# Performance work log

Measured on AMD Instinct MI355X. Metric: run time of the kernel, lower is better.

The kernel has to match this reference:

```python
import jax, jax.numpy as jnp
import numpy as np

DECAY = 0.99
EPS = 1e-05


def setup_inputs() -> dict:
    key = jax.random.key(0)
    k1, k2, k3, k4 = jax.random.split(key, 4)
    B, D, T, E = 16, 64, 4096, 1024
    x = jax.random.normal(k1, (B, D, T), dtype=jnp.float32)
    embedding = jax.random.uniform(k2, (E, D), dtype=jnp.float32,
                                   minval=-1.0 / E, maxval=1.0 / E)
    ema_size = jax.random.uniform(k3, (E,), dtype=jnp.float32)
    ema_w = jax.random.normal(k4, (D, E), dtype=jnp.float32)
    return {"x": x, "embedding": embedding, "ema_size": ema_size, "ema_w": ema_w}


def reference(x, embedding, ema_size, ema_w):
    # x: [B, D, T] (bdt_flag=True -> transpose to [B, T, D])
    B, D, T = x.shape
    E = embedding.shape[0]
    xt = jnp.swapaxes(x, 1, 2)                      # [B, T, D]
    flat = xt.reshape(-1, D)                        # [B*T, D]
    dist = (jnp.sum(embedding * embedding, axis=1)[None, :]
            - 2.0 * flat @ embedding.T
            + jnp.sum(flat * flat, axis=1, keepdims=True))  # [B*T, E]
    quantized_idx = jnp.argmin(dist, axis=1).reshape(B, T)   # [B, T] int
    onehot = jax.nn.one_hot(quantized_idx, E, dtype=x.dtype)  # [B, T, E]
    embed_idx = onehot @ embedding                  # [B, T, D]  (old codebook)
    # --- EMA codebook update (training branch) ---
    new_ema_size = DECAY * ema_size + (1.0 - DECAY) * jnp.sum(
        onehot.reshape(-1, E), axis=0)
    embed_sum = jnp.einsum('btd,bte->de', xt, onehot)        # [D, E]
    new_ema_w = DECAY * ema_w + (1.0 - DECAY) * embed_sum
    n = jnp.sum(new_ema_size)
    new_ema_size = (new_ema_size + EPS) / (n + E * EPS) * n
    new_embedding = (new_ema_w / new_ema_size[None, :]).T    # [E, D]
    # straight-through estimator
    embed_idx_qx = xt + jax.lax.stop_gradient(embed_idx - xt)
    embed_idx_qx = jnp.swapaxes(embed_idx_qx, 1, 2)          # back to [B, D, T]
    return embed_idx, embed_idx_qx, quantized_idx, new_embedding, new_ema_size, new_ema_w
```

## Files before the change

kernel.cpp:

```cpp
#include <hip/hip_runtime.h>
#include <hip/hip_bf16.h>

constexpr int Bc = 16, Dc = 64, Tc = 4096, Ec = 1024;
constexpr int NROW = Bc * Tc;
constexpr float DECAYF = 0.99f;
constexpr float OMDF   = 0.01f;
constexpr float EPSF   = 1e-5f;

typedef short bf16x8 __attribute__((ext_vector_type(8)));
typedef float f32x4  __attribute__((ext_vector_type(4)));

constexpr size_t O_EI  = 0;
constexpr size_t O_QX  = 4194304;
constexpr size_t O_IDX = 8388608;
constexpr size_t O_EMB = 8454144;
constexpr size_t O_ESZ = 8519680;
constexpr size_t O_EMW = 8520704;

constexpr size_t S_XH = 0;
constexpr size_t S_XM = 2097152;
constexpr size_t S_XL = 4194304;
constexpr size_t S_EH = 6291456;
constexpr size_t S_EM = 6324224;
constexpr size_t S_EL = 6356992;
constexpr size_t S_E2 = 6389760;
constexpr size_t S_X2 = 6424576;
constexpr size_t S_P  = 6557696;


__device__ inline unsigned short bf16bits(float v) {
  union { __hip_bfloat16 b; unsigned short u; } c;
  c.b = __float2bfloat16(v);
  return c.u;
}
__device__ inline float bf16val(unsigned short u) {
  union { unsigned u32; float f; } c;
  c.u32 = ((unsigned)u) << 16;
  return c.f;
}
__device__ inline void split3(float x, unsigned short& h, unsigned short& m,
                              unsigned short& l) {
  h = bf16bits(x);
  float r1 = x - bf16val(h);
  m = bf16bits(r1);
  float r2 = r1 - bf16val(m);
  l = bf16bits(r2);
}

__device__ inline void pack8(unsigned short* s, uint4* dst) {
  uint4 v;
  v.x = (unsigned)s[0] | ((unsigned)s[1] << 16);
  v.y = (unsigned)s[2] | ((unsigned)s[3] << 16);
  v.z = (unsigned)s[4] | ((unsigned)s[5] << 16);
  v.w = (unsigned)s[6] | ((unsigned)s[7] << 16);
  *dst = v;
}

__device__ inline void gl_lds16(const unsigned short* g, unsigned short* l) {
  __builtin_amdgcn_global_load_lds(
      (const __attribute__((address_space(1))) void*)g,
      (__attribute__((address_space(3))) void*)l, 16, 0, 0);
}

__global__ __launch_bounds__(256) void decomp_x(const float* __restrict__ x,
                                                float* __restrict__ out) {
  const int row = blockIdx.x * 256 + threadIdx.x;
  const int b = row >> 12, t = row & (Tc - 1);
  const float* xrow = x + (size_t)b * Dc * Tc + t;
  float xv[64];
  #pragma unroll
  for (int d = 0; d < Dc; ++d) xv[d] = xrow[(size_t)d * Tc];

  float x2;
  {
    #pragma clang fp contract(off)
    float r[8];
    #pragma unroll
    for (int j = 0; j < 8; ++j) r[j] = xv[j] * xv[j];
    #pragma unroll
    for (int k = 1; k < 8; ++k) {
      #pragma unroll
      for (int j = 0; j < 8; ++j) r[j] += xv[8 * k + j] * xv[8 * k + j];
    }
    x2 = ((r[0] + r[1]) + (r[2] + r[3])) + ((r[4] + r[5]) + (r[6] + r[7]));
  }
  out[S_X2 + row] = x2;

  uint4* ph = (uint4*)((unsigned short*)(out + S_XH) + (size_t)row * 64);
  uint4* pm = (uint4*)((unsigned short*)(out + S_XM) + (size_t)row * 64);
  uint4* pl = (uint4*)((unsigned short*)(out + S_XL) + (size_t)row * 64);
  #pragma unroll
  for (int k = 0; k < 8; ++k) {
    unsigned short hs[8], ms[8], ls[8];
    #pragma unroll
    for (int j = 0; j < 8; ++j) split3(xv[8 * k + j], hs[j], ms[j], ls[j]);
    pack8(hs, ph + k); pack8(ms, pm + k); pack8(ls, pl + k);
  }
}

__global__ __launch_bounds__(256) void decomp_e(const float* __restrict__ emb,
                                                float* __restrict__ out,
                                                float* __restrict__ ws) {
  const int c = blockIdx.x * 256 + threadIdx.x;
  if (c < 1024) ws[c] = 0.0f;
  if (c >= Ec) return;
  const float* ep = emb + (size_t)c * Dc;
  float ev[64];
  #pragma unroll
  for (int d = 0; d < Dc; ++d) ev[d] = ep[d];

  float e2;
  {
    #pragma clang fp contract(off)
    float r[8];
    #pragma unroll
    for (int j = 0; j < 8; ++j) r[j] = ev[j] * ev[j];
    #pragma unroll
    for (int k = 1; k < 8; ++k) {
      #pragma unroll
      for (int j = 0; j < 8; ++j) r[j] += ev[8 * k + j] * ev[8 * k + j];
    }
    e2 = ((r[0] + r[1]) + (r[2] + r[3])) + ((r[4] + r[5]) + (r[6] + r[7]));
  }
  out[S_E2 + c] = e2;

  uint4* ph = (uint4*)((unsigned short*)(out + S_EH) + (size_t)c * 64);
  uint4* pm = (uint4*)((unsigned short*)(out + S_EM) + (size_t)c * 64);
  uint4* pl = (uint4*)((unsigned short*)(out + S_EL) + (size_t)c * 64);
  #pragma unroll
  for (int k = 0; k < 8; ++k) {
    unsigned short hs[8], ms[8], ls[8];
    #pragma unroll
    for (int j = 0; j < 8; ++j) split3(ev[8 * k + j], hs[j], ms[j], ls[j]);
    pack8(hs, ph + k); pack8(ms, pm + k); pack8(ls, pl + k);
  }
}

constexpr int TW = 64;
constexpr int SLOTS = (TW / 16) * 3 * 2 * 64;

__global__ __launch_bounds__(512)
__attribute__((amdgpu_waves_per_eu(2, 2)))
void gemm_argmin(float* __restrict__ out) {
  __shared__ alignas(16) unsigned short lbuf[2][SLOTS * 8];

  const int tid  = threadIdx.x;
  const int lane = tid & 63;
  const int wave = tid >> 6;
  const int col  = lane & 15;
  const int quad = lane >> 4;
  const int rowbase = blockIdx.x * 256 + wave * 32;

  const unsigned short* XH = (const unsigned short*)(out + S_XH);
  const unsigned short* XM = (const unsigned short*)(out + S_XM);
  const unsigned short* XL = (const unsigned short*)(out + S_XL);
  const unsigned short* EHu = (const unsigned short*)(out + S_EH);
  const float* E2 = out + S_E2;
  const float* X2 = out + S_X2;

  auto stage = [&](int tl, int s) {
    #pragma unroll
    for (int i = 0; i < 3; ++i) {
      int slot = tid + i * 512;
      int sl   = slot & 63;
      int sub  = slot >> 6;
      int half = sub & 1;
      int pl   = (sub >> 1) % 3;
      int nt   = sub / 6;
      int cw   = tl * TW + nt * 16 + (sl & 15);
      int q    = sl >> 4;
      const unsigned short* src =
          EHu + (size_t)pl * 65536 + (size_t)cw * 64 + half * 32 + q * 8;
      gl_lds16(src, &lbuf[s][(size_t)slot * 8]);
    }
  };

  bf16x8 a[12];
  #pragma unroll
  for (int mt = 0; mt < 2; ++mt) {
    size_t ao = (size_t)(rowbase + mt * 16 + col) * 64 + quad * 8;
    a[mt * 6 + 0] = *(const bf16x8*)(XH + ao);
    a[mt * 6 + 1] = *(const bf16x8*)(XH + ao + 32);
    a[mt * 6 + 2] = *(const bf16x8*)(XM + ao);
    a[mt * 6 + 3] = *(const bf16x8*)(XM + ao + 32);
    a[mt * 6 + 4] = *(const bf16x8*)(XL + ao);
    a[mt * 6 + 5] = *(const bf16x8*)(XL + ao + 32);
  }
  float x2v[8];
  #pragma unroll
  for (int mt = 0; mt < 2; ++mt)
    #pragma unroll
    for (int r = 0; r < 4; ++r)
      x2v[mt * 4 + r] = X2[rowbase + mt * 16 + quad * 4 + r];

  #pragma unroll
  for (int i = 0; i < 12; ++i) asm volatile("" : "+v"(a[i]));
  #pragma unroll
  for (int i = 0; i < 8; ++i) asm volatile("" : "+v"(x2v[i]));

  float best[8];
  int bidx[8];
  #pragma unroll
  for (int i = 0; i < 8; ++i) { best[i] = 3.4e38f; bidx[i] = 0; }

  stage(0, 0);

  for (int tl = 0; tl < Ec / TW; ++tl) {
    __syncthreads();
    if (tl + 1 < Ec / TW) stage(tl + 1, (tl + 1) & 1);
    const unsigned short* lb = lbuf[tl & 1];

    #pragma unroll
    for (int np = 0; np < 2; ++np) {
      bf16x8 b0[6], b1[6];
      #pragma unroll
      for (int pl = 0; pl < 3; ++pl)
        #pragma unroll
        for (int h = 0; h < 2; ++h) {
          b0[pl * 2 + h] = *(const bf16x8*)(
              lb + ((size_t)(((((2 * np + 0) * 3 + pl) * 2 + h)) * 64 + lane)) * 8);
          b1[pl * 2 + h] = *(const bf16x8*)(
              lb + ((size_t)(((((2 * np + 1) * 3 + pl) * 2 + h)) * 64 + lane)) * 8);
        }
      const float e2v0 = E2[tl * TW + (2 * np + 0) * 16 + col];
      const float e2v1 = E2[tl * TW + (2 * np + 1) * 16 + col];

      f32x4 acc00 = {0.f, 0.f, 0.f, 0.f};
      f32x4 acc01 = {0.f, 0.f, 0.f, 0.f};
      f32x4 acc10 = {0.f, 0.f, 0.f, 0.f};
      f32x4 acc11 = {0.f, 0.f, 0.f, 0.f};
      const int PA[6] = {0, 0, 1, 1, 0, 2};
      const int PB[6] = {0, 1, 0, 1, 2, 0};
      #pragma unroll
      for (int p = 0; p < 6; ++p) {
        #pragma unroll
        for (int s = 0; s < 2; ++s) {
          bf16x8 a0 = a[PA[p] * 2 + s];
          bf16x8 a1 = a[6 + PA[p] * 2 + s];
          bf16x8 f0 = b0[PB[p] * 2 + s];
          bf16x8 f1 = b1[PB[p] * 2 + s];
          acc00 = __builtin_amdgcn_mfma_f32_16x16x32_bf16(a0, f0, acc00, 0, 0, 0);
          acc10 = __builtin_amdgcn_mfma_f32_16x16x32_bf16(a0, f1, acc10, 0, 0, 0);
          acc01 = __builtin_amdgcn_mfma_f32_16x16x32_bf16(a1, f0, acc01, 0, 0, 0);
          acc11 = __builtin_amdgcn_mfma_f32_16x16x32_bf16(a1, f1, acc11, 0, 0, 0);
        }
      }

      const int cw0 = tl * TW + (2 * np + 0) * 16 + col;
      const int cw1 = tl * TW + (2 * np + 1) * 16 + col;
      #pragma unroll
      for (int r = 0; r < 4; ++r) {
        {
          float q = __builtin_fmaf(-2.0f, acc00[r], e2v0);
          q = q + x2v[r];
          if (q < best[r]) { best[r] = q; bidx[r] = cw0; }
        }
        {
          float q = __builtin_fmaf(-2.0f, acc01[r], e2v0);
          q = q + x2v[4 + r];
          if (q < best[4 + r]) { best[4 + r] = q; bidx[4 + r] = cw0; }
        }
        {
          float q = __builtin_fmaf(-2.0f, acc10[r], e2v1);
          q = q + x2v[r];
          if (q < best[r]) { best[r] = q; bidx[r] = cw1; }
        }
        {
          float q = __builtin_fmaf(-2.0f, acc11[r], e2v1);
          q = q + x2v[4 + r];
          if (q < best[4 + r]) { best[4 + r] = q; bidx[4 + r] = cw1; }
        }
      }
    }
  }

  #pragma unroll
  for (int i = 0; i < 8; ++i) {
    float bq = best[i];
    int bi = bidx[i];
    #pragma unroll
    for (int m = 1; m <= 8; m <<= 1) {
      float qo = __shfl_xor(bq, m, 64);
      int io = __shfl_xor(bi, m, 64);
      bool take = (qo < bq) || (qo == bq && io < bi);
      bq = take ? qo : bq;
      bi = take ? io : bi;
    }
    if (col == 0) {
      int mt = i >> 2, r = i & 3;
      int row = rowbase + mt * 16 + quad * 4 + r;
      out[O_IDX + row] = (float)bi;
    }
  }
}

__global__ __launch_bounds__(512) void esum_partial(float* __restrict__ out,
                                                    float* __restrict__ ws) {
  const int c = blockIdx.x;
  const int s = blockIdx.y;
  __shared__ float acc[4 * 1025];
  __shared__ float cnt[1024];
  for (int i = threadIdx.x; i < 4 * 1025; i += 512) acc[i] = 0.f;
  if (s == 0)
    for (int i = threadIdx.x; i < 1024; i += 512) cnt[i] = 0.f;
  __syncthreads();

  const unsigned short* XH = (const unsigned short*)(out + S_XH);
  const unsigned short* XM = (const unsigned short*)(out + S_XM);
  const unsigned short* XL = (const unsigned short*)(out + S_XL);

  #pragma unroll 2
  for (int it = 0; it < 8; ++it) {
    const int r = c * 4096 + it * 512 + threadIdx.x;
    const int bi = (int)out[O_IDX + r];
    const size_t off = (size_t)r * 64 + s * 4;
    const uint2 h = *(const uint2*)(XH + off);
    const uint2 m = *(const uint2*)(XM + off);
    const uint2 l = *(const uint2*)(XL + off);

#define DOPAIR(k, HW, MW, LW)                                                  \
    {                                                                          \
      float v0 = (bf16val((unsigned short)(HW)) +                              \
                  bf16val((unsigned short)(MW))) +                             \
                 bf16val((unsigned short)(LW));                                \
      float v1 = (bf16val((unsigned short)((HW) >> 16)) +                      \
                  bf16val((unsigned short)((MW) >> 16))) +                     \
                 bf16val((unsigned short)((LW) >> 16));                        \
      atomicAdd(&acc[(2 * (k) + 0) * 1025 + bi], v0);                          \
      atomicAdd(&acc[(2 * (k) + 1) * 1025 + bi], v1);                          \
    }
    DOPAIR(0, h.x, m.x, l.x)
    DOPAIR(1, h.y, m.y, l.y)
#undef DOPAIR
    if (s == 0) atomicAdd(&cnt[bi], 1.0f);
  }
  __syncthreads();

  float* part = out + S_P + ((size_t)c * 64 + s * 4) * 1024;
  for (int i = threadIdx.x; i < 4096; i += 512)
    part[i] = acc[(i >> 10) * 1025 + (i & 1023)];
  if (s == 0)
    for (int i = threadIdx.x; i < 1024; i += 512)
      atomicAdd(&ws[i], cnt[i]);
}

__global__ __launch_bounds__(1024) void finalize_a(
    const float* __restrict__ ema_size, float* __restrict__ ws,
    float* __restrict__ out) {
  const int e = threadIdx.x;
  float ns = DECAYF * ema_size[e] + OMDF * ws[e];
  __shared__ float red[1024];
  red[e] = ns;
  __syncthreads();
  for (int s = 512; s > 0; s >>= 1) {
    if (e < s) red[e] += red[e + s];
    __syncthreads();
  }
  float n = red[0];
  float v = ((ns + EPSF) / (n + (float)Ec * EPSF)) * n;
  out[O_ESZ + e] = v;
  ws[66560 + e] = v;
}

__global__ __launch_bounds__(256) void esum_finalize_w(
    const float* __restrict__ ema_w, const float* __restrict__ ws,
    float* __restrict__ out) {
  const int i = blockIdx.x * 256 + threadIdx.x;
  float v = 0.f;
  #pragma unroll
  for (int c = 0; c < 16; ++c) v += out[S_P + (size_t)c * 65536 + i];
  int d = i >> 10;
  int e = i & (Ec - 1);
  float w = DECAYF * ema_w[i] + OMDF * v;
  out[O_EMW + i] = w;
  out[O_EMB + e * Dc + d] = w / ws[66560 + e];
}

__global__ __launch_bounds__(256) void epilogue_kernel(
    const float* __restrict__ x, const float* __restrict__ emb,
    float* __restrict__ out) {
  const int row = blockIdx.x * 256 + threadIdx.x;
  const int b = row >> 12, t = row & (Tc - 1);
  const float* xrow = x + (size_t)b * Dc * Tc + t;

  const int bi = (int)out[O_IDX + row];

  const float4* eb = (const float4*)(emb + (size_t)bi * Dc);
  float* qx_base = out + O_QX + (size_t)b * Dc * Tc + t;
  float4* ei_base = (float4*)(out + O_EI + (size_t)row * Dc);

  #pragma unroll
  for (int k = 0; k < 16; ++k) {
    float4 ev = eb[k];
    ei_base[k] = ev;
    {
      const int d = 4 * k + 0; float xd = xrow[(size_t)d * Tc];
      float diff = ev.x - xd;
      qx_base[(size_t)d * Tc] = xd + diff;
    }
    {
      const int d = 4 * k + 1; float xd = xrow[(size_t)d * Tc];
      float diff = ev.y - xd;
      qx_base[(size_t)d * Tc] = xd + diff;
    }
    {
      const int d = 4 * k + 2; float xd = xrow[(size_t)d * Tc];
      float diff = ev.z - xd;
      qx_base[(size_t)d * Tc] = xd + diff;
    }
    {
      const int d = 4 * k + 3; float xd = xrow[(size_t)d * Tc];
      float diff = ev.w - xd;
      qx_base[(size_t)d * Tc] = xd + diff;
    }
  }
}

extern "C" void kernel_launch(void* const* d_in, const int* in_sizes, int n_in,
                              void* d_out, int out_size, void* d_ws, size_t ws_size,
                              hipStream_t stream) {
  const float* x        = (const float*)d_in[0];
  const float* emb      = (const float*)d_in[1];
  const float* ema_size = (const float*)d_in[2];
  const float* ema_w    = (const float*)d_in[3];
  float* out = (float*)d_out;
  float* ws  = (float*)d_ws;

  decomp_x<<<NROW / 256, 256, 0, stream>>>(x, out);
  decomp_e<<<Ec / 256, 256, 0, stream>>>(emb, out, ws);
  gemm_argmin<<<NROW / 256, 512, 0, stream>>>(out);
  esum_partial<<<dim3(16, 16), 512, 0, stream>>>(out, ws);
  finalize_a<<<1, 1024, 0, stream>>>(ema_size, ws, out);
  esum_finalize_w<<<Ec * Dc / 256, 256, 0, stream>>>(ema_w, ws, out);
  epilogue_kernel<<<NROW / 256, 256, 0, stream>>>(x, emb, out);
}
```

Measured before the change: 187.8 us.

## Load codebook fragments directly from global into registers, dropping LDS staging

The argmin GEMM no longer stages codebook tiles into double-buffered shared memory through global_load_lds and block barriers. Each wave now loads its B fragments straight from global (L2-resident) memory into registers, with a one-step register prefetch. The block size is halved to 256 threads with 128 rows per block, so there are twice as many blocks. This removes the barriers and the LDS traffic, but every wave now reads the codebook itself, and register pressure rises from the prefetch buffers.

```diff
diff --git a/kernel.cpp b/kernel.cpp
--- a/kernel.cpp
+++ b/kernel.cpp
@@ -56,12 +56,6 @@
   *dst = v;
 }
 
-__device__ inline void gl_lds16(const unsigned short* g, unsigned short* l) {
-  __builtin_amdgcn_global_load_lds(
-      (const __attribute__((address_space(1))) void*)g,
-      (__attribute__((address_space(3))) void*)l, 16, 0, 0);
-}
-
 __global__ __launch_bounds__(256) void decomp_x(const float* __restrict__ x,
                                                 float* __restrict__ out) {
   const int row = blockIdx.x * 256 + threadIdx.x;
@@ -136,20 +130,15 @@
   }
 }
 
-constexpr int TW = 64;
-constexpr int SLOTS = (TW / 16) * 3 * 2 * 64;
-
-__global__ __launch_bounds__(512)
+__global__ __launch_bounds__(256)
 __attribute__((amdgpu_waves_per_eu(2, 2)))
 void gemm_argmin(float* __restrict__ out) {
-  __shared__ alignas(16) unsigned short lbuf[2][SLOTS * 8];
-
   const int tid  = threadIdx.x;
   const int lane = tid & 63;
   const int wave = tid >> 6;
   const int col  = lane & 15;
   const int quad = lane >> 4;
-  const int rowbase = blockIdx.x * 256 + wave * 32;
+  const int rowbase = blockIdx.x * 128 + wave * 32;
 
   const unsigned short* XH = (const unsigned short*)(out + S_XH);
   const unsigned short* XM = (const unsigned short*)(out + S_XM);
@@ -158,22 +147,7 @@
   const float* E2 = out + S_E2;
   const float* X2 = out + S_X2;
 
-  auto stage = [&](int tl, int s) {
-    #pragma unroll
-    for (int i = 0; i < 3; ++i) {
-      int slot = tid + i * 512;
-      int sl   = slot & 63;
-      int sub  = slot >> 6;
-      int half = sub & 1;
-      int pl   = (sub >> 1) % 3;
-      int nt   = sub / 6;
-      int cw   = tl * TW + nt * 16 + (sl & 15);
-      int q    = sl >> 4;
-      const unsigned short* src =
-          EHu + (size_t)pl * 65536 + (size_t)cw * 64 + half * 32 + q * 8;
-      gl_lds16(src, &lbuf[s][(size_t)slot * 8]);
-    }
-  };
+  const unsigned short* Bbase = EHu + (size_t)col * 64 + (size_t)quad * 8;
 
   bf16x8 a[12];
   #pragma unroll
@@ -203,74 +177,78 @@
   #pragma unroll
   for (int i = 0; i < 8; ++i) { best[i] = 3.4e38f; bidx[i] = 0; }
 
-  stage(0, 0);
-
-  for (int tl = 0; tl < Ec / TW; ++tl) {
-    __syncthreads();
-    if (tl + 1 < Ec / TW) stage(tl + 1, (tl + 1) & 1);
-    const unsigned short* lb = lbuf[tl & 1];
-
-    #pragma unroll
-    for (int np = 0; np < 2; ++np) {
-      bf16x8 b0[6], b1[6];
+  auto loadB = [&](int it, bf16x8* b0, bf16x8* b1) {
+    const unsigned short* p = Bbase + (size_t)it * 2048;
+    #pragma unroll
+    for (int pl = 0; pl < 3; ++pl)
       #pragma unroll
-      for (int pl = 0; pl < 3; ++pl)
-        #pragma unroll
-        for (int h = 0; h < 2; ++h) {
-          b0[pl * 2 + h] = *(const bf16x8*)(
-              lb + ((size_t)(((((2 * np + 0) * 3 + pl) * 2 + h)) * 64 + lane)) * 8);
-          b1[pl * 2 + h] = *(const bf16x8*)(
-              lb + ((size_t)(((((2 * np + 1) * 3 + pl) * 2 + h)) * 64 + lane)) * 8);
-        }
-      const float e2v0 = E2[tl * TW + (2 * np + 0) * 16 + col];
-      const float e2v1 = E2[tl * TW + (2 * np + 1) * 16 + col];
-
-      f32x4 acc00 = {0.f, 0.f, 0.f, 0.f};
-      f32x4 acc01 = {0.f, 0.f, 0.f, 0.f};
-      f32x4 acc10 = {0.f, 0.f, 0.f, 0.f};
-      f32x4 acc11 = {0.f, 0.f, 0.f, 0.f};
-      const int PA[6] = {0, 0, 1, 1, 0, 2};
-      const int PB[6] = {0, 1, 0, 1, 2, 0};
+      for (int h = 0; h < 2; ++h) {
+        b0[pl * 2 + h] = *(const bf16x8*)(p + (size_t)pl * 65536 + h * 32);
+        b1[pl * 2 + h] = *(const bf16x8*)(p + (size_t)pl * 65536 + h * 32 + 1024);
+      }
+  };
+
+  bf16x8 bc0[6], bc1[6];
+  loadB(0, bc0, bc1);
+
+  #pragma unroll 2
+  for (int it = 0; it < 32; ++it) {
+    bf16x8 bn0[6], bn1[6];
+    if (it + 1 < 32) loadB(it + 1, bn0, bn1);
+
+    const float e2v0 = E2[it * 32 + col];
+    const float e2v1 = E2[it * 32 + 16 + col];
+
+    f32x4 acc00 = {0.f, 0.f, 0.f, 0.f};
+    f32x4 acc01 = {0.f, 0.f, 0.f, 0.f};
+    f32x4 acc10 = {0.f, 0.f, 0.f, 0.f};
+    f32x4 acc11 = {0.f, 0.f, 0.f, 0.f};
+    const int PA[6] = {0, 0, 1, 1, 0, 2};
+    const int PB[6] = {0, 1, 0, 1, 2, 0};
+    #pragma unroll
+    for (int p = 0; p < 6; ++p) {
       #pragma unroll
-      for (int p = 0; p < 6; ++p) {
-        #pragma unroll
-        for (int s = 0; s < 2; ++s) {
-          bf16x8 a0 = a[PA[p] * 2 + s];
-          bf16x8 a1 = a[6 + PA[p] * 2 + s];
-          bf16x8 f0 = b0[PB[p] * 2 + s];
-          bf16x8 f1 = b1[PB[p] * 2 + s];
-          acc00 = __builtin_amdgcn_mfma_f32_16x16x32_bf16(a0, f0, acc00, 0, 0, 0);
-          acc10 = __builtin_amdgcn_mfma_f32_16x16x32_bf16(a0, f1, acc10, 0, 0, 0);
-          acc01 = __builtin_amdgcn_mfma_f32_16x16x32_bf16(a1, f0, acc01, 0, 0, 0);
-          acc11 = __builtin_amdgcn_mfma_f32_16x16x32_bf16(a1, f1, acc11, 0, 0, 0);
-        }
-      }
-
-      const int cw0 = tl * TW + (2 * np + 0) * 16 + col;
-      const int cw1 = tl * TW + (2 * np + 1) * 16 + col;
+      for (int s = 0; s < 2; ++s) {
+        bf16x8 a0 = a[PA[p] * 2 + s];
+        bf16x8 a1 = a[6 + PA[p] * 2 + s];
+        bf16x8 f0 = bc0[PB[p] * 2 + s];
+        bf16x8 f1 = bc1[PB[p] * 2 + s];
+        acc00 = __builtin_amdgcn_mfma_f32_16x16x32_bf16(a0, f0, acc00, 0, 0, 0);
+        acc10 = __builtin_amdgcn_mfma_f32_16x16x32_bf16(a0, f1, acc10, 0, 0, 0);
+        acc01 = __builtin_amdgcn_mfma_f32_16x16x32_bf16(a1, f0, acc01, 0, 0, 0);
+        acc11 = __builtin_amdgcn_mfma_f32_16x16x32_bf16(a1, f1, acc11, 0, 0, 0);
+      }
+    }
+
+    const int cw0 = it * 32 + col;
+    const int cw1 = it * 32 + 16 + col;
+    #pragma unroll
+    for (int r = 0; r < 4; ++r) {
+      {
+        float q = __builtin_fmaf(-2.0f, acc00[r], e2v0);
+        q = q + x2v[r];
+        if (q < best[r]) { best[r] = q; bidx[r] = cw0; }
+      }
+      {
+        float q = __builtin_fmaf(-2.0f, acc01[r], e2v0);
+        q = q + x2v[4 + r];
+        if (q < best[4 + r]) { best[4 + r] = q; bidx[4 + r] = cw0; }
+      }
+      {
+        float q = __builtin_fmaf(-2.0f, acc10[r], e2v1);
+        q = q + x2v[r];
+        if (q < best[r]) { best[r] = q; bidx[r] = cw1; }
+      }
+      {
+        float q = __builtin_fmaf(-2.0f, acc11[r], e2v1);
+        q = q + x2v[4 + r];
+        if (q < best[4 + r]) { best[4 + r] = q; bidx[4 + r] = cw1; }
+      }
+    }
+
+    if (it + 1 < 32) {
       #pragma unroll
-      for (int r = 0; r < 4; ++r) {
-        {
-          float q = __builtin_fmaf(-2.0f, acc00[r], e2v0);
-          q = q + x2v[r];
-          if (q < best[r]) { best[r] = q; bidx[r] = cw0; }
-        }
-        {
-          float q = __builtin_fmaf(-2.0f, acc01[r], e2v0);
-          q = q + x2v[4 + r];
-          if (q < best[4 + r]) { best[4 + r] = q; bidx[4 + r] = cw0; }
-        }
-        {
-          float q = __builtin_fmaf(-2.0f, acc10[r], e2v1);
-          q = q + x2v[r];
-          if (q < best[r]) { best[r] = q; bidx[r] = cw1; }
-        }
-        {
-          float q = __builtin_fmaf(-2.0f, acc11[r], e2v1);
-          q = q + x2v[4 + r];
-          if (q < best[4 + r]) { best[4 + r] = q; bidx[4 + r] = cw1; }
-        }
-      }
+      for (int i = 0; i < 6; ++i) { bc0[i] = bn0[i]; bc1[i] = bn1[i]; }
     }
   }
 
@@ -428,7 +406,7 @@
 
   decomp_x<<<NROW / 256, 256, 0, stream>>>(x, out);
   decomp_e<<<Ec / 256, 256, 0, stream>>>(emb, out, ws);
-  gemm_argmin<<<NROW / 256, 512, 0, stream>>>(out);
+  gemm_argmin<<<NROW / 128, 256, 0, stream>>>(out);
   esum_partial<<<dim3(16, 16), 512, 0, stream>>>(out, ws);
   finalize_a<<<1, 1024, 0, stream>>>(ema_size, ws, out);
   esum_finalize_w<<<Ec * Dc / 256, 256, 0, stream>>>(ema_w, ws, out);
```

Measured after the change: 242.6 us. +29.2%, slower.

## Split codebook range across two blocks per row tile and merge argmin later

Applied to the files above, without the earlier changes.

The distance GEMM+argmin grid is doubled so that each row tile is processed by two blocks, each scanning half of the codebook. Each block writes its best distance and index to workspace, and esum_partial merges the two halves, with ties going to the lower half, before writing the final index. The waves-per-EU hint is raised to allow more resident waves per SIMD for better latency hiding. In exchange, the X operand loads are duplicated across the two blocks, the extra partial reads and writes add memory traffic, and the higher occupancy target may force register spills.

```diff
diff --git a/kernel.cpp b/kernel.cpp
--- a/kernel.cpp
+++ b/kernel.cpp
@@ -26,6 +26,10 @@
 constexpr size_t S_E2 = 6389760;
 constexpr size_t S_X2 = 6424576;
 constexpr size_t S_P  = 6557696;
+constexpr size_t S_PB0 = 7606272;
+constexpr size_t S_PI0 = 7671808;
+constexpr size_t S_PB1 = 7737344;
+constexpr size_t S_PI1 = 7802880;
 
 
 __device__ inline unsigned short bf16bits(float v) {
@@ -137,10 +141,11 @@
 }
 
 constexpr int TW = 64;
+constexpr int NTL_H = 8;
 constexpr int SLOTS = (TW / 16) * 3 * 2 * 64;
 
 __global__ __launch_bounds__(512)
-__attribute__((amdgpu_waves_per_eu(2, 2)))
+__attribute__((amdgpu_waves_per_eu(4)))
 void gemm_argmin(float* __restrict__ out) {
   __shared__ alignas(16) unsigned short lbuf[2][SLOTS * 8];
 
@@ -149,7 +154,10 @@
   const int wave = tid >> 6;
   const int col  = lane & 15;
   const int quad = lane >> 4;
-  const int rowbase = blockIdx.x * 256 + wave * 32;
+  const int cwhalf = blockIdx.x & 1;
+  const int rowblk = blockIdx.x >> 1;
+  const int rowbase = rowblk * 256 + wave * 32;
+  const int cwbase  = cwhalf * (NTL_H * TW);
 
   const unsigned short* XH = (const unsigned short*)(out + S_XH);
   const unsigned short* XM = (const unsigned short*)(out + S_XM);
@@ -158,7 +166,7 @@
   const float* E2 = out + S_E2;
   const float* X2 = out + S_X2;
 
-  auto stage = [&](int tl, int s) {
+  auto stage = [&](int tlg, int s) {
     #pragma unroll
     for (int i = 0; i < 3; ++i) {
       int slot = tid + i * 512;
@@ -167,7 +175,7 @@
       int half = sub & 1;
       int pl   = (sub >> 1) % 3;
       int nt   = sub / 6;
-      int cw   = tl * TW + nt * 16 + (sl & 15);
+      int cw   = tlg * TW + nt * 16 + (sl & 15);
       int q    = sl >> 4;
       const unsigned short* src =
           EHu + (size_t)pl * 65536 + (size_t)cw * 64 + half * 32 + q * 8;
@@ -203,11 +211,12 @@
   #pragma unroll
   for (int i = 0; i < 8; ++i) { best[i] = 3.4e38f; bidx[i] = 0; }
 
-  stage(0, 0);
-
-  for (int tl = 0; tl < Ec / TW; ++tl) {
+  stage(cwbase / TW, 0);
+
+  for (int tl = 0; tl < NTL_H; ++tl) {
+    const int tlg = cwbase / TW + tl;
     __syncthreads();
-    if (tl + 1 < Ec / TW) stage(tl + 1, (tl + 1) & 1);
+    if (tl + 1 < NTL_H) stage(tlg + 1, (tl + 1) & 1);
     const unsigned short* lb = lbuf[tl & 1];
 
     #pragma unroll
@@ -222,8 +231,8 @@
           b1[pl * 2 + h] = *(const bf16x8*)(
               lb + ((size_t)(((((2 * np + 1) * 3 + pl) * 2 + h)) * 64 + lane)) * 8);
         }
-      const float e2v0 = E2[tl * TW + (2 * np + 0) * 16 + col];
-      const float e2v1 = E2[tl * TW + (2 * np + 1) * 16 + col];
+      const float e2v0 = E2[tlg * TW + (2 * np + 0) * 16 + col];
+      const float e2v1 = E2[tlg * TW + (2 * np + 1) * 16 + col];
 
       f32x4 acc00 = {0.f, 0.f, 0.f, 0.f};
       f32x4 acc01 = {0.f, 0.f, 0.f, 0.f};
@@ -246,8 +255,8 @@
         }
       }
 
-      const int cw0 = tl * TW + (2 * np + 0) * 16 + col;
-      const int cw1 = tl * TW + (2 * np + 1) * 16 + col;
+      const int cw0 = tlg * TW + (2 * np + 0) * 16 + col;
+      const int cw1 = tlg * TW + (2 * np + 1) * 16 + col;
       #pragma unroll
       for (int r = 0; r < 4; ++r) {
         {
@@ -274,6 +283,8 @@
     }
   }
 
+  const size_t PB = cwhalf ? S_PB1 : S_PB0;
+  const size_t PI = cwhalf ? S_PI1 : S_PI0;
   #pragma unroll
   for (int i = 0; i < 8; ++i) {
     float bq = best[i];
@@ -289,7 +300,8 @@
     if (col == 0) {
       int mt = i >> 2, r = i & 3;
       int row = rowbase + mt * 16 + quad * 4 + r;
-      out[O_IDX + row] = (float)bi;
+      out[PB + row] = bq;
+      out[PI + row] = (float)bi;
     }
   }
 }
@@ -312,7 +324,10 @@
   #pragma unroll 2
   for (int it = 0; it < 8; ++it) {
     const int r = c * 4096 + it * 512 + threadIdx.x;
-    const int bi = (int)out[O_IDX + r];
+    const float b0 = out[S_PB0 + r];
+    const float b1 = out[S_PB1 + r];
+    const int bi = (b1 < b0) ? (int)out[S_PI1 + r] : (int)out[S_PI0 + r];
+    if (s == 0) out[O_IDX + r] = (float)bi;
     const size_t off = (size_t)r * 64 + s * 4;
     const uint2 h = *(const uint2*)(XH + off);
     const uint2 m = *(const uint2*)(XM + off);
@@ -428,7 +443,7 @@
 
   decomp_x<<<NROW / 256, 256, 0, stream>>>(x, out);
   decomp_e<<<Ec / 256, 256, 0, stream>>>(emb, out, ws);
-  gemm_argmin<<<NROW / 256, 512, 0, stream>>>(out);
+  gemm_argmin<<<NROW / 128, 512, 0, stream>>>(out);
   esum_partial<<<dim3(16, 16), 512, 0, stream>>>(out, ws);
   finalize_a<<<1, 1024, 0, stream>>>(ema_size, ws, out);
   esum_finalize_w<<<Ec * Dc / 256, 256, 0, stream>>>(ema_w, ws, out);
```

Measured after the change: 276.2 us. 1.47x slower.
